# Performance work log

Measured on AMD Instinct MI355X. Metric: run time of the kernel, lower is better.

The kernel has to match this reference:

```python
import jax, jax.numpy as jnp
import numpy as np

C = 4        # num_case (3) + coreference (1)
H = 128      # self.hidden_size
D = 768      # bert hidden size
B, S = 2, 384


def setup_inputs() -> dict:
    key = jax.random.key(0)
    ks = jax.random.split(key, 9)
    sc = 0.02
    return {
        "sequence_output": jax.random.normal(ks[0], (B, S, D), jnp.float32),
        "base_score": jax.random.uniform(ks[1], (B, S, C, S), jnp.float32),
        "W_prd_w": jax.random.normal(ks[2], (D, C * H), jnp.float32) * sc,
        "W_prd_b": jnp.zeros((C * H,), jnp.float32),
        "U_arg_w": jax.random.normal(ks[3], (D, C * H), jnp.float32) * sc,
        "U_arg_b": jnp.zeros((C * H,), jnp.float32),
        "W_mid": jax.random.normal(ks[4], (H * (C + 2), H), jnp.float32) * sc,
        "b_mid": jnp.zeros((H,), jnp.float32),
        "w_out": jax.random.normal(ks[5], (H,), jnp.float32) * sc,
    }


def reference(sequence_output, base_score, W_prd_w, W_prd_b, U_arg_w, U_arg_b, W_mid, b_mid, w_out):
    b, s, _ = sequence_output.shape
    # projections (dropout = identity in eval)
    h_p = (sequence_output @ W_prd_w + W_prd_b).reshape(b, s, C, H)   # [B,S,C,H]
    h_a = (sequence_output @ U_arg_w + U_arg_b).reshape(b, s, C, H)   # [B,S,C,H]
    # weighted_sum over argument positions: base_score[b,prd,case,arg]
    ref = jnp.einsum("bach,bpca->bpch", h_a, base_score).reshape(b, s, C * H)  # [B,S,C*H]
    # mid_layer(tanh(cat[prd_rep, h_a, ref])) == sum of three block matmuls,
    # since tanh is elementwise on each concatenated block.
    W1, W2, W3 = W_mid[:H], W_mid[H:2 * H], W_mid[2 * H:]
    t_prd = jnp.einsum("bpch,hk->bpck", jnp.tanh(h_p), W1)   # [B,Sp,C,H]
    t_arg = jnp.einsum("bach,hk->back", jnp.tanh(h_a), W2)   # [B,Sa,C,H]
    t_ref = jnp.tanh(ref) @ W3                                # [B,Sp,H]
    h_mid = (t_prd[:, :, None, :, :] + t_arg[:, None, :, :, :]
             + t_ref[:, :, None, None, :] + b_mid)            # [B,Sp,Sa,C,H]
    out = jnp.tanh(h_mid) @ w_out                             # [B,Sp,Sa,C]
    return out.transpose(0, 1, 3, 2)                          # [B,Sp,C,Sa]
```

## Files before the change

kernel.cpp:

```cpp
#include <hip/hip_runtime.h>
#include <hip/hip_bf16.h>


#define C2 2.885390081777927f

typedef __attribute__((ext_vector_type(8))) __bf16 bf16x8;
typedef __attribute__((ext_vector_type(8))) unsigned short ushort8;
typedef __attribute__((ext_vector_type(4))) float float4v;

__device__ __forceinline__ unsigned short f2bf(float f) {
  unsigned int u = __float_as_uint(f);
  u += 0x7fffu + ((u >> 16) & 1u);
  return (unsigned short)(u >> 16);
}

__device__ __forceinline__ float fast_tanh(float x) {
  float e = __builtin_amdgcn_exp2f(C2 * x);
  return 1.0f - 2.0f * __builtin_amdgcn_rcpf(1.0f + e);
}

__device__ __forceinline__ void gemm_core(
    const float* __restrict__ Abase, int lda,
    const float* __restrict__ Bbase, int ldb, int K,
    unsigned short* Alds, unsigned short* Blds,
    int ar, int ac, int bk, int bn,
    int wm0, int wn0, int col16, int quad, float4v acc[2][2])
{
  const float* Ap = Abase + (size_t)ar * lda + ac;
  const float* Bp = Bbase + (size_t)bk * ldb + bn;
  float4 a0 = ((const float4*)Ap)[0], a1 = ((const float4*)Ap)[1];
  float4 b0 = ((const float4*)Bp)[0], b1 = ((const float4*)Bp)[1];

  for (int k0 = 0; k0 < K; k0 += 32) {
    __syncthreads();
    {
      ushort8 o;
      o[0] = f2bf(a0.x); o[1] = f2bf(a0.y); o[2] = f2bf(a0.z); o[3] = f2bf(a0.w);
      o[4] = f2bf(a1.x); o[5] = f2bf(a1.y); o[6] = f2bf(a1.z); o[7] = f2bf(a1.w);
      *(ushort8*)&Alds[ar * 40 + ac] = o;
      float vv[8] = {b0.x, b0.y, b0.z, b0.w, b1.x, b1.y, b1.z, b1.w};
#pragma unroll
      for (int j = 0; j < 8; ++j) Blds[(bn + j) * 40 + bk] = f2bf(vv[j]);
    }
    __syncthreads();
    if (k0 + 32 < K) {
      const float4* An = (const float4*)(Ap + k0 + 32);
      const float4* Bn = (const float4*)(Bp + (size_t)(k0 + 32) * ldb);
      a0 = An[0]; a1 = An[1]; b0 = Bn[0]; b1 = Bn[1];
    }
    bf16x8 afrag[2], bfrag[2];
#pragma unroll
    for (int i = 0; i < 2; ++i)
      afrag[i] = __builtin_bit_cast(bf16x8,
          *(const ushort8*)&Alds[(wm0 + i * 16 + col16) * 40 + quad * 8]);
#pragma unroll
    for (int j = 0; j < 2; ++j)
      bfrag[j] = __builtin_bit_cast(bf16x8,
          *(const ushort8*)&Blds[(wn0 + j * 16 + col16) * 40 + quad * 8]);
#pragma unroll
    for (int i = 0; i < 2; ++i)
#pragma unroll
      for (int j = 0; j < 2; ++j)
        acc[i][j] = __builtin_amdgcn_mfma_f32_16x16x32_bf16(
            afrag[i], bfrag[j], acc[i][j], 0, 0, 0);
  }
}

__global__ __launch_bounds__(256) void g1_dual(
    const float* __restrict__ seq, const float* __restrict__ Wp,
    const float* __restrict__ Ua, const float* __restrict__ Wpb,
    const float* __restrict__ Uab, float* __restrict__ tanh_out,
    float* __restrict__ h_a, float* __restrict__ tref_clear)
{
  const int z = blockIdx.z;
  if (z == 2) {
    int idx = ((blockIdx.y * 8 + blockIdx.x) * 256 + threadIdx.x) * 4;
    *(float4*)&tref_clear[idx] = float4{0.f, 0.f, 0.f, 0.f};
    return;
  }
  __shared__ unsigned short Alds[64 * 40];
  __shared__ unsigned short Blds[64 * 40];
  const int tid = threadIdx.x;
  const int bn0 = blockIdx.x * 64, bm0 = blockIdx.y * 64;
  const int wid = tid >> 6, lane = tid & 63;
  const int wm0 = (wid >> 1) * 32, wn0 = (wid & 1) * 32;
  const int col16 = lane & 15, quad = lane >> 4;
  const float* B = z ? Ua : Wp;
  const float* bias = z ? Uab : Wpb;

  float4v acc[2][2];
#pragma unroll
  for (int i = 0; i < 2; ++i)
#pragma unroll
    for (int j = 0; j < 2; ++j) acc[i][j] = (float4v)(0.f);

  gemm_core(seq + (size_t)bm0 * 768, 768, B + bn0, 512, 768,
            Alds, Blds, tid >> 2, (tid & 3) * 8, tid >> 3, (tid & 7) * 8,
            wm0, wn0, col16, quad, acc);

  float* tout = tanh_out + (size_t)z * 393216;
#pragma unroll
  for (int j = 0; j < 2; ++j) {
    const int gcol = bn0 + wn0 + j * 16 + col16;
    const float bv = bias[gcol];
#pragma unroll
    for (int i = 0; i < 2; ++i)
#pragma unroll
      for (int r = 0; r < 4; ++r) {
        const int grow = bm0 + wm0 + i * 16 + quad * 4 + r;
        const float x = acc[i][j][r] + bv;
        const size_t cidx = (size_t)grow * 512 + gcol;
        tout[cidx] = fast_tanh(x);
        if (z == 1) h_a[cidx] = x;
      }
  }
}

__global__ __launch_bounds__(256) void fused_mid(
    const float* __restrict__ base, const float* __restrict__ h_a,
    const float* __restrict__ tanh_h, const float* __restrict__ Wmid,
    float* __restrict__ tprd_s, unsigned short* __restrict__ targ_s,
    float* __restrict__ tref_s)
{
  __shared__ unsigned short Alds[64 * 40];
  __shared__ unsigned short Blds[64 * 40];
  __shared__ unsigned short TA[64 * 72];
  __shared__ unsigned short TB[128 * 72];

  const int tid = threadIdx.x;
  const int bid = blockIdx.x;
  const int wid = tid >> 6, lane = tid & 63;
  const int wm0 = (wid >> 1) * 32, wn0 = (wid & 1) * 32;
  const int col16 = lane & 15, quad = lane >> 4;
  const int ar = tid >> 2, ac = (tid & 3) * 8;
  const int bk = tid >> 3, bn = (tid & 7) * 8;

  float4v acc[2][2];
#pragma unroll
  for (int i = 0; i < 2; ++i)
#pragma unroll
    for (int j = 0; j < 2; ++j) acc[i][j] = (float4v)(0.f);

  if (bid < 96) {
    const int z = bid / 12, rem = bid % 12;
    const int b = z >> 2, c = z & 3;
    const int y = rem >> 1, x = rem & 1;
    const float* A = base + (size_t)b * 589824 + c * 384 + (size_t)(y * 64) * 1536;
    const float* Bm = h_a + (size_t)b * 196608 + c * 128 + x * 64;
    gemm_core(A, 1536, Bm, 512, 384, Alds, Blds, ar, ac, bk, bn,
              wm0, wn0, col16, quad, acc);

#pragma unroll
    for (int j = 0; j < 2; ++j)
#pragma unroll
      for (int i = 0; i < 2; ++i)
#pragma unroll
        for (int r = 0; r < 4; ++r)
          TA[(wm0 + i * 16 + quad * 4 + r) * 72 + wn0 + j * 16 + col16] =
              f2bf(fast_tanh(acc[i][j][r]));
    {
      const float* W3p = Wmid + 32768 + (size_t)(c * 128 + x * 64) * 128;
      const int kr = tid >> 2, nb = (tid & 3) * 32;
#pragma unroll
      for (int q = 0; q < 8; ++q) {
        float4 v = *(const float4*)(W3p + (size_t)kr * 128 + nb + q * 4);
        TB[(nb + q * 4 + 0) * 72 + kr] = f2bf(v.x);
        TB[(nb + q * 4 + 1) * 72 + kr] = f2bf(v.y);
        TB[(nb + q * 4 + 2) * 72 + kr] = f2bf(v.z);
        TB[(nb + q * 4 + 3) * 72 + kr] = f2bf(v.w);
      }
    }
    __syncthreads();

    const int mh = wid & 1, nh = wid >> 1;
    float4v acc2[2][4];
#pragma unroll
    for (int i = 0; i < 2; ++i)
#pragma unroll
      for (int j = 0; j < 4; ++j) acc2[i][j] = (float4v)(0.f);
#pragma unroll
    for (int ks = 0; ks < 2; ++ks) {
      bf16x8 af[2], bf[4];
#pragma unroll
      for (int i = 0; i < 2; ++i)
        af[i] = __builtin_bit_cast(bf16x8,
            *(const ushort8*)&TA[(mh * 32 + i * 16 + col16) * 72 + ks * 32 + quad * 8]);
#pragma unroll
      for (int j = 0; j < 4; ++j)
        bf[j] = __builtin_bit_cast(bf16x8,
            *(const ushort8*)&TB[(nh * 64 + j * 16 + col16) * 72 + ks * 32 + quad * 8]);
#pragma unroll
      for (int i = 0; i < 2; ++i)
#pragma unroll
        for (int j = 0; j < 4; ++j)
          acc2[i][j] = __builtin_amdgcn_mfma_f32_16x16x32_bf16(
              af[i], bf[j], acc2[i][j], 0, 0, 0);
    }
#pragma unroll
    for (int j = 0; j < 4; ++j) {
      const int gcol = nh * 64 + j * 16 + col16;
#pragma unroll
      for (int i = 0; i < 2; ++i)
#pragma unroll
        for (int r = 0; r < 4; ++r) {
          const int grow = b * 384 + y * 64 + mh * 32 + i * 16 + quad * 4 + r;
          atomicAdd(&tref_s[(size_t)grow * 128 + gcol], C2 * acc2[i][j][r]);
        }
    }
  } else {
    const int idx = bid - 96;
    const int x = idx & 1, y = (idx >> 1) % 48, z = idx / 96;
    const float* A = tanh_h + (size_t)z * 393216 + (size_t)(y * 64) * 128;
    const float* Bm = Wmid + z * 16384 + x * 64;
    gemm_core(A, 128, Bm, 128, 128, Alds, Blds, ar, ac, bk, bn,
              wm0, wn0, col16, quad, acc);
#pragma unroll
    for (int j = 0; j < 2; ++j) {
      const int gcol = x * 64 + wn0 + j * 16 + col16;
#pragma unroll
      for (int i = 0; i < 2; ++i)
#pragma unroll
        for (int r = 0; r < 4; ++r) {
          const int grow = y * 64 + wm0 + i * 16 + quad * 4 + r;
          const float v = C2 * acc[i][j][r];
          const size_t cidx = (size_t)grow * 128 + gcol;
          if (z == 0) tprd_s[cidx] = v;
          else        targ_s[cidx] = f2bf(v);
        }
    }
  }
}

__global__ __launch_bounds__(256) void phase2(
    const float* __restrict__ tprd, const unsigned short* __restrict__ targ,
    const float* __restrict__ tref, const float* __restrict__ bmid,
    const float* __restrict__ wout, float* __restrict__ out)
{
  __shared__ float Es[8 * 128];
  __shared__ float Ws[128];
  __shared__ float Red[128 * 9];

  const int tid = threadIdx.x;
  const int a = tid & 127, kh = tid >> 7;
  const int p0 = blockIdx.x * 8, a0 = blockIdx.y * 128;
  const int b = blockIdx.z >> 2, c = blockIdx.z & 3;

  const uint4* grow = (const uint4*)((const unsigned int*)targ +
      (size_t)((b * 384 + a0 + a) * 4 + c) * 64 + kh * 32);
  uint4 G[8];
#pragma unroll
  for (int i = 0; i < 8; ++i) G[i] = grow[i];

  if (tid < 128) Ws[tid] = -2.f * wout[tid];
#pragma unroll
  for (int it = 0; it < 4; ++it) {
    int idx = it * 256 + tid;
    int p = idx >> 7, k = idx & 127;
    int row = b * 384 + p0 + p;
    Es[idx] = __builtin_amdgcn_exp2f(
        tprd[(size_t)(row * 4 + c) * 128 + k] +
        tref[(size_t)row * 128 + k] + C2 * bmid[k]);
  }
  float sw = 0.f;
  for (int k4 = 0; k4 < 32; ++k4) {
    float4 w = ((const float4*)wout)[k4];
    sw += w.x + w.y + w.z + w.w;
  }
  __syncthreads();

  float acc[8];
#pragma unroll
  for (int p = 0; p < 8; ++p) acc[p] = 0.f;

  const int kb0 = kh * 64;
#pragma unroll
  for (int j = 0; j < 8; ++j) {
    const uint4 gq = G[j];
    const float eg0 = __builtin_amdgcn_exp2f(__uint_as_float(gq.x << 16));
    const float eg1 = __builtin_amdgcn_exp2f(__uint_as_float(gq.x & 0xffff0000u));
    const float eg2 = __builtin_amdgcn_exp2f(__uint_as_float(gq.y << 16));
    const float eg3 = __builtin_amdgcn_exp2f(__uint_as_float(gq.y & 0xffff0000u));
    const float eg4 = __builtin_amdgcn_exp2f(__uint_as_float(gq.z << 16));
    const float eg5 = __builtin_amdgcn_exp2f(__uint_as_float(gq.z & 0xffff0000u));
    const float eg6 = __builtin_amdgcn_exp2f(__uint_as_float(gq.w << 16));
    const float eg7 = __builtin_amdgcn_exp2f(__uint_as_float(gq.w & 0xffff0000u));
    const int kb = kb0 + j * 8;
    const float4 wqA = *(const float4*)&Ws[kb];
    const float4 wqB = *(const float4*)&Ws[kb + 4];
#pragma unroll
    for (int p = 0; p < 8; ++p) {
      const float4 efA = *(const float4*)&Es[p * 128 + kb];
      const float4 efB = *(const float4*)&Es[p * 128 + kb + 4];
      float d0 = fmaf(efA.x, eg0, 1.f);
      float d1 = fmaf(efA.y, eg1, 1.f);
      float d2 = fmaf(efA.z, eg2, 1.f);
      float d3 = fmaf(efA.w, eg3, 1.f);
      float d01 = d0 * d1, d23 = d2 * d3;
      float n01 = fmaf(wqA.y, d0, wqA.x * d1);
      float n23 = fmaf(wqA.w, d2, wqA.z * d3);
      float num = fmaf(n01, d23, n23 * d01);
      acc[p] = fmaf(num, __builtin_amdgcn_rcpf(d01 * d23), acc[p]);
      d0 = fmaf(efB.x, eg4, 1.f);
      d1 = fmaf(efB.y, eg5, 1.f);
      d2 = fmaf(efB.z, eg6, 1.f);
      d3 = fmaf(efB.w, eg7, 1.f);
      d01 = d0 * d1; d23 = d2 * d3;
      n01 = fmaf(wqB.y, d0, wqB.x * d1);
      n23 = fmaf(wqB.w, d2, wqB.z * d3);
      num = fmaf(n01, d23, n23 * d01);
      acc[p] = fmaf(num, __builtin_amdgcn_rcpf(d01 * d23), acc[p]);
    }
  }

  if (kh) {
#pragma unroll
    for (int p = 0; p < 8; ++p) Red[a * 9 + p] = acc[p];
  }
  __syncthreads();
  if (!kh) {
    const size_t ob = (size_t)((b * 384 + p0) * 4 + c) * 384 + a0 + a;
#pragma unroll
    for (int p = 0; p < 8; ++p)
      out[ob + (size_t)p * 1536] = sw + acc[p] + Red[a * 9 + p];
  }
}

extern "C" void kernel_launch(void* const* d_in, const int* in_sizes, int n_in,
                              void* d_out, int out_size, void* d_ws, size_t ws_size,
                              hipStream_t stream) {
  (void)in_sizes; (void)n_in; (void)out_size; (void)ws_size;
  const float* seq  = (const float*)d_in[0];
  const float* base = (const float*)d_in[1];
  const float* Wp   = (const float*)d_in[2];
  const float* Wpb  = (const float*)d_in[3];
  const float* Ua   = (const float*)d_in[4];
  const float* Uab  = (const float*)d_in[5];
  const float* Wmid = (const float*)d_in[6];
  const float* bmid = (const float*)d_in[7];
  const float* wout = (const float*)d_in[8];
  float* out = (float*)d_out;

  float* ws = (float*)d_ws;
  float* tanh_h = ws;
  float* h_a    = ws + 786432;
  float* tprd_s = ws + 1179648;
  float* tref_s = ws + 1572864;
  unsigned short* targ_s = (unsigned short*)(ws + 1671168);

  g1_dual<<<dim3(8, 12, 3), dim3(256), 0, stream>>>(
      seq, Wp, Ua, Wpb, Uab, tanh_h, h_a, tref_s);
  fused_mid<<<dim3(288), dim3(256), 0, stream>>>(
      base, h_a, tanh_h, Wmid, tprd_s, targ_s, tref_s);
  phase2<<<dim3(48, 3, 8), dim3(256), 0, stream>>>(
      tprd_s, targ_s, tref_s, bmid, wout, out);
}
```

Before: 132.9 us.

## Split-K GEMMs across two thread groups, store bf16 intermediates, drop atomics

Doubles block size to 512 threads and splits each GEMM's K dimension between two 256-thread groups, reducing their partial results through shared memory. Intermediates tanh(h) and h_a are now stored as bf16, with h_a transposed so the weighted-sum GEMM can load B tiles with plain vector loads. The atomicAdd accumulation into tref, along with the zeroing pass it needed, is replaced by eight separate partial buffers that phase2 sums on the fly. This adds an extra reduction step, more shared-memory traffic, and extra reads in phase2, and it changes the LDS row stride.

```diff
diff --git a/kernel.cpp b/kernel.cpp
--- a/kernel.cpp
+++ b/kernel.cpp
@@ -3,6 +3,8 @@
 
 
 #define C2 2.885390081777927f
+#define LSH 42
+#define LSZ (64 * LSH)
 
 typedef __attribute__((ext_vector_type(8))) __bf16 bf16x8;
 typedef __attribute__((ext_vector_type(8))) unsigned short ushort8;
@@ -19,44 +21,72 @@
   return 1.0f - 2.0f * __builtin_amdgcn_rcpf(1.0f + e);
 }
 
+template <int AF, int BF>
 __device__ __forceinline__ void gemm_core(
-    const float* __restrict__ Abase, int lda,
-    const float* __restrict__ Bbase, int ldb, int K,
+    const void* __restrict__ Abase, int lda,
+    const void* __restrict__ Bbase, int ldb, int K,
     unsigned short* Alds, unsigned short* Blds,
-    int ar, int ac, int bk, int bn,
-    int wm0, int wn0, int col16, int quad, float4v acc[2][2])
+    int t, int g, int wm0, int wn0, int col16, int quad, float4v acc[2][2])
 {
-  const float* Ap = Abase + (size_t)ar * lda + ac;
-  const float* Bp = Bbase + (size_t)bk * ldb + bn;
-  float4 a0 = ((const float4*)Ap)[0], a1 = ((const float4*)Ap)[1];
-  float4 b0 = ((const float4*)Bp)[0], b1 = ((const float4*)Bp)[1];
-
-  for (int k0 = 0; k0 < K; k0 += 32) {
+  const int Kh = K >> 1;
+  const int ar = t >> 2, ac = (t & 3) * 8;
+  const int bk = t >> 3, bn = (t & 7) * 8;
+
+  const float* Afp = (const float*)Abase + (size_t)ar * lda + g * Kh + ac;
+  const unsigned short* Abp =
+      (const unsigned short*)Abase + (size_t)ar * lda + g * Kh + ac;
+  const float* Bfp = (const float*)Bbase + (size_t)(g * Kh + bk) * ldb + bn;
+  const unsigned short* Bbp =
+      (const unsigned short*)Bbase + (size_t)ar * ldb + g * Kh + ac;
+
+  float4 a0, a1, b0, b1;
+  ushort8 a16, b16;
+  if constexpr (AF == 0) { a0 = ((const float4*)Afp)[0]; a1 = ((const float4*)Afp)[1]; }
+  else                   { a16 = *(const ushort8*)Abp; }
+  if constexpr (BF == 0) { b0 = ((const float4*)Bfp)[0]; b1 = ((const float4*)Bfp)[1]; }
+  else                   { b16 = *(const ushort8*)Bbp; }
+
+  for (int k0 = 0; k0 < Kh; k0 += 32) {
     __syncthreads();
-    {
+    if constexpr (AF == 0) {
       ushort8 o;
       o[0] = f2bf(a0.x); o[1] = f2bf(a0.y); o[2] = f2bf(a0.z); o[3] = f2bf(a0.w);
       o[4] = f2bf(a1.x); o[5] = f2bf(a1.y); o[6] = f2bf(a1.z); o[7] = f2bf(a1.w);
-      *(ushort8*)&Alds[ar * 40 + ac] = o;
+      *(ushort8*)&Alds[ar * LSH + ac] = o;
+    } else {
+      *(ushort8*)&Alds[ar * LSH + ac] = a16;
+    }
+    if constexpr (BF == 0) {
       float vv[8] = {b0.x, b0.y, b0.z, b0.w, b1.x, b1.y, b1.z, b1.w};
 #pragma unroll
-      for (int j = 0; j < 8; ++j) Blds[(bn + j) * 40 + bk] = f2bf(vv[j]);
+      for (int j = 0; j < 8; ++j) Blds[(bn + j) * LSH + bk] = f2bf(vv[j]);
+    } else {
+      *(ushort8*)&Blds[ar * LSH + ac] = b16;
     }
     __syncthreads();
-    if (k0 + 32 < K) {
-      const float4* An = (const float4*)(Ap + k0 + 32);
-      const float4* Bn = (const float4*)(Bp + (size_t)(k0 + 32) * ldb);
-      a0 = An[0]; a1 = An[1]; b0 = Bn[0]; b1 = Bn[1];
+    if (k0 + 32 < Kh) {
+      if constexpr (AF == 0) {
+        const float4* An = (const float4*)(Afp + k0 + 32);
+        a0 = An[0]; a1 = An[1];
+      } else {
+        a16 = *(const ushort8*)(Abp + k0 + 32);
+      }
+      if constexpr (BF == 0) {
+        const float4* Bn = (const float4*)(Bfp + (size_t)(k0 + 32) * ldb);
+        b0 = Bn[0]; b1 = Bn[1];
+      } else {
+        b16 = *(const ushort8*)(Bbp + k0 + 32);
+      }
     }
     bf16x8 afrag[2], bfrag[2];
 #pragma unroll
     for (int i = 0; i < 2; ++i)
       afrag[i] = __builtin_bit_cast(bf16x8,
-          *(const ushort8*)&Alds[(wm0 + i * 16 + col16) * 40 + quad * 8]);
+          *(const ushort8*)&Alds[(wm0 + i * 16 + col16) * LSH + quad * 8]);
 #pragma unroll
     for (int j = 0; j < 2; ++j)
       bfrag[j] = __builtin_bit_cast(bf16x8,
-          *(const ushort8*)&Blds[(wn0 + j * 16 + col16) * 40 + quad * 8]);
+          *(const ushort8*)&Blds[(wn0 + j * 16 + col16) * LSH + quad * 8]);
 #pragma unroll
     for (int i = 0; i < 2; ++i)
 #pragma unroll
@@ -66,27 +96,46 @@
   }
 }
 
-__global__ __launch_bounds__(256) void g1_dual(
+__device__ __forceinline__ void reduce_groups(float4v acc[2][2], float* scratch,
+                                              int tid) {
+  __syncthreads();
+  if (tid >= 256) {
+    float* s = scratch + (tid - 256) * 20;
+#pragma unroll
+    for (int i = 0; i < 2; ++i)
+#pragma unroll
+      for (int j = 0; j < 2; ++j)
+        *(float4v*)&s[(i * 2 + j) * 4] = acc[i][j];
+  }
+  __syncthreads();
+  if (tid < 256) {
+    const float* s = scratch + tid * 20;
+#pragma unroll
+    for (int i = 0; i < 2; ++i)
+#pragma unroll
+      for (int j = 0; j < 2; ++j)
+        acc[i][j] += *(const float4v*)&s[(i * 2 + j) * 4];
+  }
+}
+
+__global__ __launch_bounds__(512) void g1_dual(
     const float* __restrict__ seq, const float* __restrict__ Wp,
     const float* __restrict__ Ua, const float* __restrict__ Wpb,
-    const float* __restrict__ Uab, float* __restrict__ tanh_out,
-    float* __restrict__ h_a, float* __restrict__ tref_clear)
+    const float* __restrict__ Uab, unsigned short* __restrict__ tanh16,
+    unsigned short* __restrict__ haT)
 {
+  __shared__ unsigned short AB[4 * LSZ];
+  const int tid = threadIdx.x;
   const int z = blockIdx.z;
-  if (z == 2) {
-    int idx = ((blockIdx.y * 8 + blockIdx.x) * 256 + threadIdx.x) * 4;
-    *(float4*)&tref_clear[idx] = float4{0.f, 0.f, 0.f, 0.f};
-    return;
-  }
-  __shared__ unsigned short Alds[64 * 40];
-  __shared__ unsigned short Blds[64 * 40];
-  const int tid = threadIdx.x;
   const int bn0 = blockIdx.x * 64, bm0 = blockIdx.y * 64;
-  const int wid = tid >> 6, lane = tid & 63;
-  const int wm0 = (wid >> 1) * 32, wn0 = (wid & 1) * 32;
+  const int g = tid >> 8, t = tid & 255;
+  const int wid2 = (tid >> 6) & 3, lane = tid & 63;
+  const int wm0 = (wid2 >> 1) * 32, wn0 = (wid2 & 1) * 32;
   const int col16 = lane & 15, quad = lane >> 4;
   const float* B = z ? Ua : Wp;
   const float* bias = z ? Uab : Wpb;
+  unsigned short* Alds = AB + (g * 2) * LSZ;
+  unsigned short* Blds = AB + (g * 2 + 1) * LSZ;
 
   float4v acc[2][2];
 #pragma unroll
@@ -94,46 +143,57 @@
 #pragma unroll
     for (int j = 0; j < 2; ++j) acc[i][j] = (float4v)(0.f);
 
-  gemm_core(seq + (size_t)bm0 * 768, 768, B + bn0, 512, 768,
-            Alds, Blds, tid >> 2, (tid & 3) * 8, tid >> 3, (tid & 7) * 8,
-            wm0, wn0, col16, quad, acc);
-
-  float* tout = tanh_out + (size_t)z * 393216;
-#pragma unroll
-  for (int j = 0; j < 2; ++j) {
-    const int gcol = bn0 + wn0 + j * 16 + col16;
-    const float bv = bias[gcol];
-#pragma unroll
-    for (int i = 0; i < 2; ++i)
-#pragma unroll
-      for (int r = 0; r < 4; ++r) {
-        const int grow = bm0 + wm0 + i * 16 + quad * 4 + r;
-        const float x = acc[i][j][r] + bv;
-        const size_t cidx = (size_t)grow * 512 + gcol;
-        tout[cidx] = fast_tanh(x);
-        if (z == 1) h_a[cidx] = x;
-      }
-  }
-}
-
-__global__ __launch_bounds__(256) void fused_mid(
-    const float* __restrict__ base, const float* __restrict__ h_a,
-    const float* __restrict__ tanh_h, const float* __restrict__ Wmid,
+  gemm_core<0, 0>(seq + (size_t)bm0 * 768, 768, B + bn0, 512, 768,
+                  Alds, Blds, t, g, wm0, wn0, col16, quad, acc);
+  reduce_groups(acc, (float*)AB, tid);
+
+  if (tid < 256) {
+    unsigned short* tout = tanh16 + (size_t)z * 393216;
+#pragma unroll
+    for (int j = 0; j < 2; ++j) {
+      const int gcol = bn0 + wn0 + j * 16 + col16;
+      const float bv = bias[gcol];
+#pragma unroll
+      for (int i = 0; i < 2; ++i) {
+        const int grow0 = bm0 + wm0 + i * 16 + quad * 4;
+        float x[4];
+#pragma unroll
+        for (int r = 0; r < 4; ++r) x[r] = acc[i][j][r] + bv;
+#pragma unroll
+        for (int r = 0; r < 4; ++r)
+          tout[(size_t)(grow0 + r) * 512 + gcol] = f2bf(fast_tanh(x[r]));
+        if (z == 1) {
+          const int bb = grow0 >= 384 ? 1 : 0;
+          const int a0 = grow0 - bb * 384;
+          const int cc = gcol >> 7, hh = gcol & 127;
+          uint2 pk;
+          pk.x = (unsigned)f2bf(x[0]) | ((unsigned)f2bf(x[1]) << 16);
+          pk.y = (unsigned)f2bf(x[2]) | ((unsigned)f2bf(x[3]) << 16);
+          *(uint2*)&haT[(size_t)((bb * 4 + cc) * 128 + hh) * 384 + a0] = pk;
+        }
+      }
+    }
+  }
+}
+
+__global__ __launch_bounds__(512) void fused_mid(
+    const float* __restrict__ base, const unsigned short* __restrict__ haT,
+    const unsigned short* __restrict__ tanh16, const float* __restrict__ Wmid,
     float* __restrict__ tprd_s, unsigned short* __restrict__ targ_s,
-    float* __restrict__ tref_s)
+    float* __restrict__ tref_part)
 {
-  __shared__ unsigned short Alds[64 * 40];
-  __shared__ unsigned short Blds[64 * 40];
+  __shared__ unsigned short AB[4 * LSZ];
   __shared__ unsigned short TA[64 * 72];
   __shared__ unsigned short TB[128 * 72];
 
   const int tid = threadIdx.x;
   const int bid = blockIdx.x;
-  const int wid = tid >> 6, lane = tid & 63;
-  const int wm0 = (wid >> 1) * 32, wn0 = (wid & 1) * 32;
+  const int g = tid >> 8, t = tid & 255;
+  const int wid2 = (tid >> 6) & 3, lane = tid & 63;
+  const int wm0 = (wid2 >> 1) * 32, wn0 = (wid2 & 1) * 32;
   const int col16 = lane & 15, quad = lane >> 4;
-  const int ar = tid >> 2, ac = (tid & 3) * 8;
-  const int bk = tid >> 3, bn = (tid & 7) * 8;
+  unsigned short* Alds = AB + (g * 2) * LSZ;
+  unsigned short* Blds = AB + (g * 2 + 1) * LSZ;
 
   float4v acc[2][2];
 #pragma unroll
@@ -142,27 +202,31 @@
     for (int j = 0; j < 2; ++j) acc[i][j] = (float4v)(0.f);
 
   if (bid < 96) {
-    const int z = bid / 12, rem = bid % 12;
-    const int b = z >> 2, c = z & 3;
+    const int zz = bid / 12, rem = bid % 12;
+    const int b = zz >> 2, c = zz & 3;
     const int y = rem >> 1, x = rem & 1;
     const float* A = base + (size_t)b * 589824 + c * 384 + (size_t)(y * 64) * 1536;
-    const float* Bm = h_a + (size_t)b * 196608 + c * 128 + x * 64;
-    gemm_core(A, 1536, Bm, 512, 384, Alds, Blds, ar, ac, bk, bn,
-              wm0, wn0, col16, quad, acc);
-
-#pragma unroll
-    for (int j = 0; j < 2; ++j)
-#pragma unroll
-      for (int i = 0; i < 2; ++i)
-#pragma unroll
-        for (int r = 0; r < 4; ++r)
-          TA[(wm0 + i * 16 + quad * 4 + r) * 72 + wn0 + j * 16 + col16] =
-              f2bf(fast_tanh(acc[i][j][r]));
+    const unsigned short* Bm =
+        haT + (size_t)((b * 4 + c) * 128 + x * 64) * 384;
+    gemm_core<0, 1>(A, 1536, Bm, 384, 384, Alds, Blds, t, g,
+                    wm0, wn0, col16, quad, acc);
+    reduce_groups(acc, (float*)AB, tid);
+
+    if (tid < 256) {
+#pragma unroll
+      for (int j = 0; j < 2; ++j)
+#pragma unroll
+        for (int i = 0; i < 2; ++i)
+#pragma unroll
+          for (int r = 0; r < 4; ++r)
+            TA[(wm0 + i * 16 + quad * 4 + r) * 72 + wn0 + j * 16 + col16] =
+                f2bf(fast_tanh(acc[i][j][r]));
+    }
     {
       const float* W3p = Wmid + 32768 + (size_t)(c * 128 + x * 64) * 128;
-      const int kr = tid >> 2, nb = (tid & 3) * 32;
-#pragma unroll
-      for (int q = 0; q < 8; ++q) {
+      const int kr = tid >> 3, nb = (tid & 7) * 16;
+#pragma unroll
+      for (int q = 0; q < 4; ++q) {
         float4 v = *(const float4*)(W3p + (size_t)kr * 128 + nb + q * 4);
         TB[(nb + q * 4 + 0) * 72 + kr] = f2bf(v.x);
         TB[(nb + q * 4 + 1) * 72 + kr] = f2bf(v.y);
@@ -172,61 +236,67 @@
     }
     __syncthreads();
 
-    const int mh = wid & 1, nh = wid >> 1;
-    float4v acc2[2][4];
-#pragma unroll
-    for (int i = 0; i < 2; ++i)
-#pragma unroll
-      for (int j = 0; j < 4; ++j) acc2[i][j] = (float4v)(0.f);
-#pragma unroll
-    for (int ks = 0; ks < 2; ++ks) {
-      bf16x8 af[2], bf[4];
+    if (tid < 256) {
+      const int mh = wid2 & 1, nh = wid2 >> 1;
+      float4v acc2[2][4];
 #pragma unroll
       for (int i = 0; i < 2; ++i)
-        af[i] = __builtin_bit_cast(bf16x8,
-            *(const ushort8*)&TA[(mh * 32 + i * 16 + col16) * 72 + ks * 32 + quad * 8]);
-#pragma unroll
-      for (int j = 0; j < 4; ++j)
-        bf[j] = __builtin_bit_cast(bf16x8,
-            *(const ushort8*)&TB[(nh * 64 + j * 16 + col16) * 72 + ks * 32 + quad * 8]);
-#pragma unroll
-      for (int i = 0; i < 2; ++i)
+#pragma unroll
+        for (int j = 0; j < 4; ++j) acc2[i][j] = (float4v)(0.f);
+#pragma unroll
+      for (int ks = 0; ks < 2; ++ks) {
+        bf16x8 af[2], bf[4];
+#pragma unroll
+        for (int i = 0; i < 2; ++i)
+          af[i] = __builtin_bit_cast(bf16x8,
+              *(const ushort8*)&TA[(mh * 32 + i * 16 + col16) * 72 + ks * 32 + quad * 8]);
 #pragma unroll
         for (int j = 0; j < 4; ++j)
-          acc2[i][j] = __builtin_amdgcn_mfma_f32_16x16x32_bf16(
-              af[i], bf[j], acc2[i][j], 0, 0, 0);
-    }
-#pragma unroll
-    for (int j = 0; j < 4; ++j) {
-      const int gcol = nh * 64 + j * 16 + col16;
-#pragma unroll
-      for (int i = 0; i < 2; ++i)
-#pragma unroll
-        for (int r = 0; r < 4; ++r) {
-          const int grow = b * 384 + y * 64 + mh * 32 + i * 16 + quad * 4 + r;
-          atomicAdd(&tref_s[(size_t)grow * 128 + gcol], C2 * acc2[i][j][r]);
-        }
+          bf[j] = __builtin_bit_cast(bf16x8,
+              *(const ushort8*)&TB[(nh * 64 + j * 16 + col16) * 72 + ks * 32 + quad * 8]);
+#pragma unroll
+        for (int i = 0; i < 2; ++i)
+#pragma unroll
+          for (int j = 0; j < 4; ++j)
+            acc2[i][j] = __builtin_amdgcn_mfma_f32_16x16x32_bf16(
+                af[i], bf[j], acc2[i][j], 0, 0, 0);
+      }
+      float* outp = tref_part + (size_t)(c * 2 + x) * 98304;
+#pragma unroll
+      for (int j = 0; j < 4; ++j) {
+        const int gcol = nh * 64 + j * 16 + col16;
+#pragma unroll
+        for (int i = 0; i < 2; ++i)
+#pragma unroll
+          for (int r = 0; r < 4; ++r) {
+            const int grow = b * 384 + y * 64 + mh * 32 + i * 16 + quad * 4 + r;
+            outp[(size_t)grow * 128 + gcol] = C2 * acc2[i][j][r];
+          }
+      }
     }
   } else {
     const int idx = bid - 96;
     const int x = idx & 1, y = (idx >> 1) % 48, z = idx / 96;
-    const float* A = tanh_h + (size_t)z * 393216 + (size_t)(y * 64) * 128;
+    const unsigned short* A = tanh16 + (size_t)z * 393216 + (size_t)(y * 64) * 128;
     const float* Bm = Wmid + z * 16384 + x * 64;
-    gemm_core(A, 128, Bm, 128, 128, Alds, Blds, ar, ac, bk, bn,
-              wm0, wn0, col16, quad, acc);
-#pragma unroll
-    for (int j = 0; j < 2; ++j) {
-      const int gcol = x * 64 + wn0 + j * 16 + col16;
-#pragma unroll
-      for (int i = 0; i < 2; ++i)
-#pragma unroll
-        for (int r = 0; r < 4; ++r) {
-          const int grow = y * 64 + wm0 + i * 16 + quad * 4 + r;
-          const float v = C2 * acc[i][j][r];
-          const size_t cidx = (size_t)grow * 128 + gcol;
-          if (z == 0) tprd_s[cidx] = v;
-          else        targ_s[cidx] = f2bf(v);
-        }
+    gemm_core<1, 0>(A, 128, Bm, 128, 128, Alds, Blds, t, g,
+                    wm0, wn0, col16, quad, acc);
+    reduce_groups(acc, (float*)AB, tid);
+    if (tid < 256) {
+#pragma unroll
+      for (int j = 0; j < 2; ++j) {
+        const int gcol = x * 64 + wn0 + j * 16 + col16;
+#pragma unroll
+        for (int i = 0; i < 2; ++i)
+#pragma unroll
+          for (int r = 0; r < 4; ++r) {
+            const int grow = y * 64 + wm0 + i * 16 + quad * 4 + r;
+            const float v = C2 * acc[i][j][r];
+            const size_t cidx = (size_t)grow * 128 + gcol;
+            if (z == 0) tprd_s[cidx] = v;
+            else        targ_s[cidx] = f2bf(v);
+          }
+      }
     }
   }
 }
@@ -257,9 +327,11 @@
     int idx = it * 256 + tid;
     int p = idx >> 7, k = idx & 127;
     int row = b * 384 + p0 + p;
+    const float* tr = tref + (size_t)row * 128 + k;
+    float s8 = tr[0] + tr[98304] + tr[2 * 98304] + tr[3 * 98304] +
+               tr[4 * 98304] + tr[5 * 98304] + tr[6 * 98304] + tr[7 * 98304];
     Es[idx] = __builtin_amdgcn_exp2f(
-        tprd[(size_t)(row * 4 + c) * 128 + k] +
-        tref[(size_t)row * 128 + k] + C2 * bmid[k]);
+        tprd[(size_t)(row * 4 + c) * 128 + k] + s8 + C2 * bmid[k]);
   }
   float sw = 0.f;
   for (int k4 = 0; k4 < 32; ++k4) {
@@ -341,16 +413,16 @@
   float* out = (float*)d_out;
 
   float* ws = (float*)d_ws;
-  float* tanh_h = ws;
-  float* h_a    = ws + 786432;
-  float* tprd_s = ws + 1179648;
-  float* tref_s = ws + 1572864;
-  unsigned short* targ_s = (unsigned short*)(ws + 1671168);
-
-  g1_dual<<<dim3(8, 12, 3), dim3(256), 0, stream>>>(
-      seq, Wp, Ua, Wpb, Uab, tanh_h, h_a, tref_s);
-  fused_mid<<<dim3(288), dim3(256), 0, stream>>>(
-      base, h_a, tanh_h, Wmid, tprd_s, targ_s, tref_s);
+  unsigned short* tanh16 = (unsigned short*)ws;
+  unsigned short* haT    = (unsigned short*)(ws + 393216);
+  float* tprd_s          = ws + 589824;
+  unsigned short* targ_s = (unsigned short*)(ws + 983040);
+  float* tref_part       = ws + 1179648;
+
+  g1_dual<<<dim3(8, 12, 2), dim3(512), 0, stream>>>(
+      seq, Wp, Ua, Wpb, Uab, tanh16, haT);
+  fused_mid<<<dim3(288), dim3(512), 0, stream>>>(
+      base, haT, tanh16, Wmid, tprd_s, targ_s, tref_part);
   phase2<<<dim3(48, 3, 8), dim3(256), 0, stream>>>(
-      tprd_s, targ_s, tref_s, bmid, wout, out);
-}
+      tprd_s, targ_s, tref_part, bmid, wout, out);
+}
```

After: 134.7 us. No clear change (+1.4%).
